# Performance work log

Measured on AMD Instinct MI355X. Metric: run time of the kernel, lower is better.

Reference implementation:

```python
import jax, jax.numpy as jnp
import numpy as np

KEY_DIM = 32
D = 128  # attn_ratio * key_dim
H = 8
DIM = 512
N = 1024
B = 16
EPS = 1e-5


def setup_inputs() -> dict:
    key = jax.random.key(0)
    ks = jax.random.split(key, 5)
    x = jax.random.normal(ks[0], (B, DIM, N), dtype=jnp.float32)
    # grouped Conv1d(dim -> H*(2*key_dim+d), k=1, groups=H): per-group weight [H, 192, 64]
    qkv_w = jax.random.normal(ks[1], (H, 2 * KEY_DIM + D, DIM // H), dtype=jnp.float32) * 0.05
    qkv_b = jax.random.normal(ks[2], (H, 2 * KEY_DIM + D), dtype=jnp.float32) * 0.02
    # proj Conv1d(d*H -> dim, k=1)
    proj_w = jax.random.normal(ks[3], (DIM, D * H), dtype=jnp.float32) * 0.03
    proj_b = jax.random.normal(ks[4], (DIM,), dtype=jnp.float32) * 0.02
    bn_gamma = jnp.ones((DIM,), dtype=jnp.float32)
    bn_beta = jnp.zeros((DIM,), dtype=jnp.float32)
    bn_mean = jnp.zeros((DIM,), dtype=jnp.float32)
    bn_var = jnp.ones((DIM,), dtype=jnp.float32)
    return {"x": x, "qkv_w": qkv_w, "qkv_b": qkv_b, "proj_w": proj_w,
            "proj_b": proj_b, "bn_gamma": bn_gamma, "bn_beta": bn_beta,
            "bn_mean": bn_mean, "bn_var": bn_var}


def reference(x, qkv_w, qkv_b, proj_w, proj_b, bn_gamma, bn_beta, bn_mean, bn_var):
    Bx, C, Nx = x.shape
    scale = KEY_DIM ** (-0.5)
    # grouped 1x1 conv: split channels into H groups of C//H
    xh = x.reshape(Bx, H, C // H, Nx)                      # [B,H,Cg,N]
    qkv = jnp.einsum('bhcn,hoc->bhon', xh, qkv_w) + qkv_b[None, :, :, None]
    q, k, v = jnp.split(qkv, [KEY_DIM, 2 * KEY_DIM], axis=2)  # [B,H,kd,N],[B,H,kd,N],[B,H,d,N]
    # attn[m,n] = sum_c q[c,m]*k[c,n]
    attn = jnp.einsum('bhcm,bhcn->bhmn', q, k) * scale      # [B,H,N,N]
    attn = jax.nn.softmax(attn, axis=-1)
    # out[d,m] = sum_n v[d,n]*attn[m,n]  (v @ attn^T)
    o = jnp.einsum('bhdn,bhmn->bhdm', v, attn)              # [B,H,d,N]
    o = o.reshape(Bx, H * D, Nx)
    # proj: ReLU -> 1x1 conv -> BatchNorm1d (inference mode)
    o = jax.nn.relu(o)
    o = jnp.einsum('bcn,oc->bon', o, proj_w) + proj_b[None, :, None]
    inv = bn_gamma / jnp.sqrt(bn_var + EPS)
    o = o * inv[None, :, None] + (bn_beta - bn_mean * inv)[None, :, None]
    return o
```

## Files before the change

### kernel.cpp

```cpp
#include <hip/hip_runtime.h>
#include <math.h>

typedef unsigned short u16;
typedef unsigned int u32;

#define Bb   16
#define Hh   8
#define KD   32
#define DV   128
#define DIM  512
#define Nn   1024
#define OQKV 192
#define SCALE2 0.25503490221320355f

typedef short bf16x8 __attribute__((ext_vector_type(8)));
typedef float f32x16 __attribute__((ext_vector_type(16)));

#define MFMA32(a, b, c) __builtin_amdgcn_mfma_f32_32x32x16_bf16(a, b, c, 0, 0, 0)

__device__ __forceinline__ float fexp2(float x) {
#if __has_builtin(__builtin_amdgcn_exp2f)
  return __builtin_amdgcn_exp2f(x);
#else
  return exp2f(x);
#endif
}

__device__ __forceinline__ u16 f2bf_rn(float f) {
  return (u16)((__float_as_uint(f) + 0x8000u) >> 16);
}

#if __has_builtin(__builtin_amdgcn_cvt_pk_bf16_f32)
__device__ __forceinline__ u32 pk2(float lo, float hi) {
  auto r = __builtin_amdgcn_cvt_pk_bf16_f32(lo, hi);
  return __builtin_bit_cast(u32, r);
}
#else
__device__ __forceinline__ u32 pk2(float lo, float hi) {
  u32 a = __float_as_uint(lo) + 0x8000u;
  u32 b = __float_as_uint(hi) + 0x8000u;
  return __builtin_amdgcn_perm(b, a, 0x07060302);
}
#endif

#if __has_builtin(__builtin_amdgcn_permlane32_swap)
__device__ __forceinline__ void pswap(u32& a, u32& b) {
  auto r = __builtin_amdgcn_permlane32_swap(a, b, false, false);
  a = r[0]; b = r[1];
}
#else
__device__ __forceinline__ void pswap(u32& a, u32& b) {
  asm("v_permlane32_swap_b32 %0, %1" : "+v"(a), "+v"(b));
}
#endif

__global__ __launch_bounds__(256) void prep_kernel(
    const float* __restrict__ pw, const float* __restrict__ qw,
    const float* __restrict__ pb, const float* __restrict__ g,
    const float* __restrict__ bt, const float* __restrict__ mn,
    const float* __restrict__ vr, u16* __restrict__ Wb,
    u16* __restrict__ Wq, float* __restrict__ invA, float* __restrict__ addB) {
  const int tid = blockIdx.x * 256 + threadIdx.x;
  {
    float4 v = *(const float4*)&pw[(size_t)tid * 4];
    uint2 pk; pk.x = pk2(v.x, v.y); pk.y = pk2(v.z, v.w);
    *(uint2*)&Wb[(size_t)tid * 4] = pk;
  }
  if (tid < 24576) {
    float4 v = *(const float4*)&qw[(size_t)tid * 4];
    uint2 pk; pk.x = pk2(v.x, v.y); pk.y = pk2(v.z, v.w);
    *(uint2*)&Wq[(size_t)tid * 4] = pk;
  }
  if (tid < DIM) {
    float inv = g[tid] * rsqrtf(vr[tid] + 1e-5f);
    invA[tid] = inv;
    addB[tid] = pb[tid] * inv + bt[tid] - mn[tid] * inv;
  }
}

__global__ __launch_bounds__(256) void qkv_kernel(
    const float* __restrict__ x, const u16* __restrict__ Wq,
    const float* __restrict__ bias, u16* __restrict__ Qb,
    u16* __restrict__ Kb, u16* __restrict__ Vb) {
  const int nt = blockIdx.x, bh = blockIdx.y;
  const int b = bh >> 3, h = bh & 7;
  const int tid = threadIdx.x;
  const int wid = tid >> 6, lane = tid & 63;
  const int r32 = lane & 31, hh = lane >> 5;
  const int n0 = nt * 128;

  __shared__ __align__(16) u16 Ws[192 * 72];
  __shared__ __align__(16) u16 Xs[128 * 72];

  const u16* wqp = Wq + (size_t)h * OQKV * 64;
  #pragma unroll
  for (int i = 0; i < 6; ++i) {
    int idx = i * 256 + tid;
    int o = idx >> 3, c8 = (idx & 7) * 8;
    *(uint4*)&Ws[o * 72 + c8] = *(const uint4*)&wqp[o * 64 + c8];
  }
  const float* xp = x + ((size_t)b * DIM + h * 64) * Nn + n0;
  #pragma unroll
  for (int i = 0; i < 4; ++i) {
    int idx = i * 256 + tid;
    int cp = idx >> 5, n4 = (idx & 31) * 4;
    const int c = 2 * cp;
    float4 a = *(const float4*)&xp[(size_t)c * Nn + n4];
    float4 d = *(const float4*)&xp[(size_t)(c + 1) * Nn + n4];
    *(u32*)&Xs[(n4 + 0) * 72 + c] = pk2(a.x, d.x);
    *(u32*)&Xs[(n4 + 1) * 72 + c] = pk2(a.y, d.y);
    *(u32*)&Xs[(n4 + 2) * 72 + c] = pk2(a.z, d.z);
    *(u32*)&Xs[(n4 + 3) * 72 + c] = pk2(a.w, d.w);
  }
  __syncthreads();

  f32x16 acc[6];
  #pragma unroll
  for (int t = 0; t < 6; ++t)
    #pragma unroll
    for (int r = 0; r < 16; ++r) acc[t][r] = 0.0f;

  const int nw = wid * 32;
  #pragma unroll
  for (int k = 0; k < 4; ++k) {
    const int ko = k * 16 + hh * 8;
    bf16x8 xb = *(const bf16x8*)&Xs[(nw + r32) * 72 + ko];
    #pragma unroll
    for (int t = 0; t < 6; ++t) {
      bf16x8 wa = *(const bf16x8*)&Ws[(t * 32 + r32) * 72 + ko];
      acc[t] = MFMA32(wa, xb, acc[t]);
    }
  }

  const int n = n0 + nw + r32;
  const float* bp = bias + h * OQKV;
  #pragma unroll
  for (int t = 0; t < 6; ++t) {
    #pragma unroll
    for (int g = 0; g < 4; ++g) {
      const int ob = t * 32 + 8 * g + 4 * hh;
      float4 bv = *(const float4*)&bp[ob];
      float v0 = acc[t][4 * g + 0] + bv.x;
      float v1 = acc[t][4 * g + 1] + bv.y;
      float v2 = acc[t][4 * g + 2] + bv.z;
      float v3 = acc[t][4 * g + 3] + bv.w;
      if (t == 0) {
        uint2 pk;
        pk.x = pk2(v0 * SCALE2, v1 * SCALE2);
        pk.y = pk2(v2 * SCALE2, v3 * SCALE2);
        *(uint2*)&Qb[((size_t)bh * Nn + n) * 32 + ob] = pk;
      } else if (t == 1) {
        uint2 pk; pk.x = pk2(v0, v1); pk.y = pk2(v2, v3);
        *(uint2*)&Kb[((size_t)bh * Nn + n) * 32 + ob - 32] = pk;
      } else {
        const int d = ob - 64;
        Vb[((size_t)bh * DV + d + 0) * Nn + n] = f2bf_rn(v0);
        Vb[((size_t)bh * DV + d + 1) * Nn + n] = f2bf_rn(v1);
        Vb[((size_t)bh * DV + d + 2) * Nn + n] = f2bf_rn(v2);
        Vb[((size_t)bh * DV + d + 3) * Nn + n] = f2bf_rn(v3);
      }
    }
  }
}

__global__ __launch_bounds__(256) void attn_kernel(
    const u16* __restrict__ Qb, const u16* __restrict__ Kb,
    const u16* __restrict__ Vb, u16* __restrict__ Ot) {
  const int blk = blockIdx.x;
  const int xcd = blk & 7, j = blk >> 3;
  const int bh = (xcd << 4) | (j >> 3);
  const int mt = j & 7;
  const int tid = threadIdx.x;
  const int wid = tid >> 6, lane = tid & 63;
  const int r32 = lane & 31, hh = lane >> 5;
  const int mw = mt * 128 + wid * 32;

  __shared__ __align__(16) u16 Vs[2][128 * 72];

  const u16* qp = Qb + ((size_t)bh * Nn + mw + r32) * 32;
  const bf16x8 qb0 = *(const bf16x8*)&qp[hh * 8];
  const bf16x8 qb1 = *(const bf16x8*)&qp[16 + hh * 8];

  const u16* kbase = Kb + (size_t)bh * Nn * 32;
  const u16* vbase = Vb + (size_t)bh * DV * Nn;

  int sd[4], sn[4];
  #pragma unroll
  for (int i = 0; i < 4; ++i) {
    int idx = i * 256 + tid;
    sd[i] = idx >> 3; sn[i] = (idx & 7) * 8;
  }

  uint4 vreg[4];
  #pragma unroll
  for (int i = 0; i < 4; ++i)
    vreg[i] = *(const uint4*)&vbase[(size_t)sd[i] * Nn + sn[i]];
  #pragma unroll
  for (int i = 0; i < 4; ++i)
    *(uint4*)&Vs[0][sd[i] * 72 + sn[i]] = vreg[i];

  bf16x8 ka[4];
  {
    const u16* kp0 = kbase + (size_t)r32 * 32;
    const u16* kp1 = kbase + (size_t)(32 + r32) * 32;
    ka[0] = *(const bf16x8*)&kp0[hh * 8];
    ka[1] = *(const bf16x8*)&kp0[16 + hh * 8];
    ka[2] = *(const bf16x8*)&kp1[hh * 8];
    ka[3] = *(const bf16x8*)&kp1[16 + hh * 8];
  }

  f32x16 o[4];
  #pragma unroll
  for (int t = 0; t < 4; ++t)
    #pragma unroll
    for (int r = 0; r < 16; ++r) o[t][r] = 0.0f;
  float lsum = 0.0f;

  for (int ch = 0; ch < 16; ++ch) {
    const int n0 = ch * 64;
    const int p = ch & 1;
    __syncthreads();

    if (ch < 15) {
      #pragma unroll
      for (int i = 0; i < 4; ++i)
        vreg[i] = *(const uint4*)&vbase[(size_t)sd[i] * Nn + n0 + 64 + sn[i]];
    }

    f32x16 c0, c1;
    #pragma unroll
    for (int r = 0; r < 16; ++r) { c0[r] = 0.0f; c1[r] = 0.0f; }
    __builtin_amdgcn_s_setprio(1);
    c0 = MFMA32(ka[0], qb0, c0);
    c0 = MFMA32(ka[1], qb1, c0);
    c1 = MFMA32(ka[2], qb0, c1);
    c1 = MFMA32(ka[3], qb1, c1);
    __builtin_amdgcn_s_setprio(0);

    bf16x8 kn[4];
    if (ch < 15) {
      const u16* kp0 = kbase + (size_t)(n0 + 64 + r32) * 32;
      const u16* kp1 = kbase + (size_t)(n0 + 96 + r32) * 32;
      kn[0] = *(const bf16x8*)&kp0[hh * 8];
      kn[1] = *(const bf16x8*)&kp0[16 + hh * 8];
      kn[2] = *(const bf16x8*)&kp1[hh * 8];
      kn[3] = *(const bf16x8*)&kp1[16 + hh * 8];
    }

    float csum = 0.0f;
    #pragma unroll
    for (int r = 0; r < 16; ++r) { c0[r] = fexp2(c0[r]); csum += c0[r]; }
    #pragma unroll
    for (int r = 0; r < 16; ++r) { c1[r] = fexp2(c1[r]); csum += c1[r]; }
    lsum += csum;

    u32 Pk[16];
    #pragma unroll
    for (int g = 0; g < 4; ++g) {
      Pk[2 * g]     = pk2(c0[4 * g + 0], c0[4 * g + 1]);
      Pk[2 * g + 1] = pk2(c0[4 * g + 2], c0[4 * g + 3]);
      Pk[8 + 2 * g]     = pk2(c1[4 * g + 0], c1[4 * g + 1]);
      Pk[8 + 2 * g + 1] = pk2(c1[4 * g + 2], c1[4 * g + 3]);
    }
    pswap(Pk[0], Pk[2]);   pswap(Pk[1], Pk[3]);
    pswap(Pk[4], Pk[6]);   pswap(Pk[5], Pk[7]);
    pswap(Pk[8], Pk[10]);  pswap(Pk[9], Pk[11]);
    pswap(Pk[12], Pk[14]); pswap(Pk[13], Pk[15]);

    union { u32 d[4]; bf16x8 v; } pb[4];
    #pragma unroll
    for (int i = 0; i < 4; ++i) {
      pb[i].d[0] = Pk[4 * i + 0];
      pb[i].d[1] = Pk[4 * i + 1];
      pb[i].d[2] = Pk[4 * i + 2];
      pb[i].d[3] = Pk[4 * i + 3];
    }

    __builtin_amdgcn_s_setprio(1);
    #pragma unroll
    for (int t = 0; t < 4; ++t) {
      const u16* vrow = &Vs[p][(t * 32 + r32) * 72];
      #pragma unroll
      for (int s = 0; s < 4; ++s) {
        bf16x8 va = *(const bf16x8*)&vrow[s * 16 + hh * 8];
        o[t] = MFMA32(va, pb[s].v, o[t]);
      }
    }
    __builtin_amdgcn_s_setprio(0);

    if (ch < 15) {
      #pragma unroll
      for (int i = 0; i < 4; ++i)
        *(uint4*)&Vs[1 - p][sd[i] * 72 + sn[i]] = vreg[i];
      #pragma unroll
      for (int i = 0; i < 4; ++i) ka[i] = kn[i];
    }
  }

  lsum += __shfl_xor(lsum, 32, 64);
  const float inv = 1.0f / lsum;
  const int m = mw + r32;
  const int b = bh >> 3, h = bh & 7;
  u16* obase = Ot + ((size_t)b * Nn + m) * 1024 + h * DV + 4 * hh;
  #pragma unroll
  for (int t = 0; t < 4; ++t) {
    #pragma unroll
    for (int g = 0; g < 4; ++g) {
      float v0 = fmaxf(o[t][4 * g + 0] * inv, 0.0f);
      float v1 = fmaxf(o[t][4 * g + 1] * inv, 0.0f);
      float v2 = fmaxf(o[t][4 * g + 2] * inv, 0.0f);
      float v3 = fmaxf(o[t][4 * g + 3] * inv, 0.0f);
      uint2 pk; pk.x = pk2(v0, v1); pk.y = pk2(v2, v3);
      *(uint2*)&obase[t * 32 + 8 * g] = pk;
    }
  }
}

__global__ __launch_bounds__(256) void proj_kernel(
    const u16* __restrict__ Ot, const u16* __restrict__ Wb,
    const float* __restrict__ invA, const float* __restrict__ addB,
    float* __restrict__ out) {
  const int blk = blockIdx.x;
  const int xcd = blk & 7, rr = blk >> 3;
  const int pairl = rr >> 2, oct = rr & 3;
  const int pair = xcd * 16 + pairl;
  const int b = pair >> 3, nt = pair & 7;
  const int n0 = nt * 128, oc0 = oct * 128;
  const int tid = threadIdx.x;
  const int wid = tid >> 6, lane = tid & 63;
  const int r32 = lane & 31, hh = lane >> 5;
  const int ocw = (wid >> 1) * 64, nw = (wid & 1) * 64;

  __shared__ __align__(16) u16 Ws[128 * 72];
  __shared__ __align__(16) u16 Os[128 * 72];

  f32x16 o[2][2];
  #pragma unroll
  for (int t = 0; t < 2; ++t)
    #pragma unroll
    for (int u = 0; u < 2; ++u)
      #pragma unroll
      for (int r = 0; r < 16; ++r) o[t][u][r] = 0.0f;

  for (int ic0 = 0; ic0 < 1024; ic0 += 64) {
    __syncthreads();
    #pragma unroll
    for (int i = 0; i < 4; ++i) {
      int idx = i * 256 + tid;
      int row = idx >> 3, c8 = (idx & 7) * 8;
      *(uint4*)&Ws[row * 72 + c8] =
          *(const uint4*)&Wb[(size_t)(oc0 + row) * 1024 + ic0 + c8];
    }
    #pragma unroll
    for (int i = 0; i < 4; ++i) {
      int idx = i * 256 + tid;
      int row = idx >> 3, c8 = (idx & 7) * 8;
      *(uint4*)&Os[row * 72 + c8] =
          *(const uint4*)&Ot[((size_t)b * Nn + n0 + row) * 1024 + ic0 + c8];
    }
    __syncthreads();

    #pragma unroll
    for (int s = 0; s < 4; ++s) {
      const int ko = s * 16 + hh * 8;
      bf16x8 a0 = *(const bf16x8*)&Ws[(ocw + r32) * 72 + ko];
      bf16x8 a1 = *(const bf16x8*)&Ws[(ocw + 32 + r32) * 72 + ko];
      bf16x8 b0 = *(const bf16x8*)&Os[(nw + r32) * 72 + ko];
      bf16x8 b1 = *(const bf16x8*)&Os[(nw + 32 + r32) * 72 + ko];
      o[0][0] = MFMA32(a0, b0, o[0][0]);
      o[0][1] = MFMA32(a0, b1, o[0][1]);
      o[1][0] = MFMA32(a1, b0, o[1][0]);
      o[1][1] = MFMA32(a1, b1, o[1][1]);
    }
  }

  #pragma unroll
  for (int t = 0; t < 2; ++t) {
    const int obase = oc0 + ocw + t * 32 + 4 * hh;
    #pragma unroll
    for (int g = 0; g < 4; ++g) {
      const int oc = obase + 8 * g;
      float4 iv = *(const float4*)&invA[oc];
      float4 av = *(const float4*)&addB[oc];
      #pragma unroll
      for (int u = 0; u < 2; ++u) {
        const int n = n0 + nw + u * 32 + r32;
        out[((size_t)b * DIM + oc + 0) * Nn + n] = o[t][u][4 * g + 0] * iv.x + av.x;
        out[((size_t)b * DIM + oc + 1) * Nn + n] = o[t][u][4 * g + 1] * iv.y + av.y;
        out[((size_t)b * DIM + oc + 2) * Nn + n] = o[t][u][4 * g + 2] * iv.z + av.z;
        out[((size_t)b * DIM + oc + 3) * Nn + n] = o[t][u][4 * g + 3] * iv.w + av.w;
      }
    }
  }
}

extern "C" void kernel_launch(void* const* d_in, const int* in_sizes, int n_in,
                              void* d_out, int out_size, void* d_ws,
                              size_t ws_size, hipStream_t stream) {
  const float* x      = (const float*)d_in[0];
  const float* qkv_w  = (const float*)d_in[1];
  const float* qkv_b  = (const float*)d_in[2];
  const float* proj_w = (const float*)d_in[3];
  const float* proj_b = (const float*)d_in[4];
  const float* bn_g   = (const float*)d_in[5];
  const float* bn_b   = (const float*)d_in[6];
  const float* bn_m   = (const float*)d_in[7];
  const float* bn_v   = (const float*)d_in[8];
  float* out = (float*)d_out;

  char* ws = (char*)d_ws;
  u16* Qb   = (u16*)(ws);
  u16* Kb   = (u16*)(ws + 8388608);
  u16* Vb   = (u16*)(ws + 16777216);
  u16* Ot   = (u16*)(ws + 50331648);
  u16* Wb   = (u16*)(ws + 83886080);
  u16* Wq   = (u16*)(ws + 84934656);
  float* invA = (float*)(ws + 85131264);
  float* addB = (float*)(ws + 85133312);

  prep_kernel<<<dim3(512), 256, 0, stream>>>(
      proj_w, qkv_w, proj_b, bn_g, bn_b, bn_m, bn_v, Wb, Wq, invA, addB);
  qkv_kernel<<<dim3(8, Bb * Hh), 256, 0, stream>>>(x, Wq, qkv_b, Qb, Kb, Vb);
  attn_kernel<<<dim3(1024), 256, 0, stream>>>(Qb, Kb, Vb, Ot);
  proj_kernel<<<dim3(512), 256, 0, stream>>>(Ot, Wb, invA, addB, out);
}
```

Baseline: 190.8 us.

## Software-pipeline QK^T and exp of next chunk against PV MFMAs

Restructures the attention loop so the QK^T MFMAs and exp/pack of chunk ch+1 are issued alongside the PV MFMAs of chunk ch. The first S tile is computed in a prologue and the last PV pass runs in an epilogue. The aim is to hide the softmax VALU work and the dependent MFMA latency behind matrix work. The cost is more live registers (the packed P tile stays resident). The last iteration also prefetches K rows past N, which are never used but may read out of bounds for the final head.

Measured after the change: 188.3 us. Within noise of the previous version (-1.3%).

```diff
diff --git a/kernel.cpp b/kernel.cpp
--- a/kernel.cpp
+++ b/kernel.cpp
@@ -208,6 +208,22 @@
     ka[2] = *(const bf16x8*)&kp1[hh * 8];
     ka[3] = *(const bf16x8*)&kp1[16 + hh * 8];
   }
+  f32x16 c0, c1;
+  #pragma unroll
+  for (int r = 0; r < 16; ++r) { c0[r] = 0.0f; c1[r] = 0.0f; }
+  c0 = MFMA32(ka[0], qb0, c0);
+  c0 = MFMA32(ka[1], qb1, c0);
+  c1 = MFMA32(ka[2], qb0, c1);
+  c1 = MFMA32(ka[3], qb1, c1);
+
+  {
+    const u16* kp0 = kbase + (size_t)(64 + r32) * 32;
+    const u16* kp1 = kbase + (size_t)(96 + r32) * 32;
+    ka[0] = *(const bf16x8*)&kp0[hh * 8];
+    ka[1] = *(const bf16x8*)&kp0[16 + hh * 8];
+    ka[2] = *(const bf16x8*)&kp1[hh * 8];
+    ka[3] = *(const bf16x8*)&kp1[16 + hh * 8];
+  }
 
   f32x16 o[4];
   #pragma unroll
@@ -215,46 +231,16 @@
     #pragma unroll
     for (int r = 0; r < 16; ++r) o[t][r] = 0.0f;
   float lsum = 0.0f;
-
-  for (int ch = 0; ch < 16; ++ch) {
-    const int n0 = ch * 64;
-    const int p = ch & 1;
-    __syncthreads();
-
-    if (ch < 15) {
-      #pragma unroll
-      for (int i = 0; i < 4; ++i)
-        vreg[i] = *(const uint4*)&vbase[(size_t)sd[i] * Nn + n0 + 64 + sn[i]];
-    }
-
-    f32x16 c0, c1;
-    #pragma unroll
-    for (int r = 0; r < 16; ++r) { c0[r] = 0.0f; c1[r] = 0.0f; }
-    __builtin_amdgcn_s_setprio(1);
-    c0 = MFMA32(ka[0], qb0, c0);
-    c0 = MFMA32(ka[1], qb1, c0);
-    c1 = MFMA32(ka[2], qb0, c1);
-    c1 = MFMA32(ka[3], qb1, c1);
-    __builtin_amdgcn_s_setprio(0);
-
-    bf16x8 kn[4];
-    if (ch < 15) {
-      const u16* kp0 = kbase + (size_t)(n0 + 64 + r32) * 32;
-      const u16* kp1 = kbase + (size_t)(n0 + 96 + r32) * 32;
-      kn[0] = *(const bf16x8*)&kp0[hh * 8];
-      kn[1] = *(const bf16x8*)&kp0[16 + hh * 8];
-      kn[2] = *(const bf16x8*)&kp1[hh * 8];
-      kn[3] = *(const bf16x8*)&kp1[16 + hh * 8];
-    }
-
+  u32 Pk[16];
+  union { u32 d[4]; bf16x8 v; } pbf[4];
+
+  auto finishS = [&]() {
     float csum = 0.0f;
     #pragma unroll
     for (int r = 0; r < 16; ++r) { c0[r] = fexp2(c0[r]); csum += c0[r]; }
     #pragma unroll
     for (int r = 0; r < 16; ++r) { c1[r] = fexp2(c1[r]); csum += c1[r]; }
     lsum += csum;
-
-    u32 Pk[16];
     #pragma unroll
     for (int g = 0; g < 4; ++g) {
       Pk[2 * g]     = pk2(c0[4 * g + 0], c0[4 * g + 1]);
@@ -266,36 +252,76 @@
     pswap(Pk[4], Pk[6]);   pswap(Pk[5], Pk[7]);
     pswap(Pk[8], Pk[10]);  pswap(Pk[9], Pk[11]);
     pswap(Pk[12], Pk[14]); pswap(Pk[13], Pk[15]);
-
-    union { u32 d[4]; bf16x8 v; } pb[4];
     #pragma unroll
     for (int i = 0; i < 4; ++i) {
-      pb[i].d[0] = Pk[4 * i + 0];
-      pb[i].d[1] = Pk[4 * i + 1];
-      pb[i].d[2] = Pk[4 * i + 2];
-      pb[i].d[3] = Pk[4 * i + 3];
-    }
+      pbf[i].d[0] = Pk[4 * i + 0];
+      pbf[i].d[1] = Pk[4 * i + 1];
+      pbf[i].d[2] = Pk[4 * i + 2];
+      pbf[i].d[3] = Pk[4 * i + 3];
+    }
+  };
+
+  finishS();
+
+  for (int ch = 0; ch < 15; ++ch) {
+    const int p = ch & 1;
+    __syncthreads();
+
+    #pragma unroll
+    for (int i = 0; i < 4; ++i)
+      vreg[i] = *(const uint4*)&vbase[(size_t)sd[i] * Nn + (ch + 1) * 64 + sn[i]];
 
     __builtin_amdgcn_s_setprio(1);
+    #pragma unroll
+    for (int r = 0; r < 16; ++r) { c0[r] = 0.0f; c1[r] = 0.0f; }
+    c0 = MFMA32(ka[0], qb0, c0);
+    c0 = MFMA32(ka[1], qb1, c0);
+    c1 = MFMA32(ka[2], qb0, c1);
+    c1 = MFMA32(ka[3], qb1, c1);
+
+    bf16x8 kn[4];
+    {
+      const u16* kp0 = kbase + (size_t)((ch + 2) * 64 + r32) * 32;
+      const u16* kp1 = kbase + (size_t)((ch + 2) * 64 + 32 + r32) * 32;
+      kn[0] = *(const bf16x8*)&kp0[hh * 8];
+      kn[1] = *(const bf16x8*)&kp0[16 + hh * 8];
+      kn[2] = *(const bf16x8*)&kp1[hh * 8];
+      kn[3] = *(const bf16x8*)&kp1[16 + hh * 8];
+    }
+
     #pragma unroll
     for (int t = 0; t < 4; ++t) {
       const u16* vrow = &Vs[p][(t * 32 + r32) * 72];
       #pragma unroll
       for (int s = 0; s < 4; ++s) {
         bf16x8 va = *(const bf16x8*)&vrow[s * 16 + hh * 8];
-        o[t] = MFMA32(va, pb[s].v, o[t]);
+        o[t] = MFMA32(va, pbf[s].v, o[t]);
       }
     }
     __builtin_amdgcn_s_setprio(0);
 
-    if (ch < 15) {
-      #pragma unroll
-      for (int i = 0; i < 4; ++i)
-        *(uint4*)&Vs[1 - p][sd[i] * 72 + sn[i]] = vreg[i];
-      #pragma unroll
-      for (int i = 0; i < 4; ++i) ka[i] = kn[i];
-    }
-  }
+    #pragma unroll
+    for (int i = 0; i < 4; ++i)
+      *(uint4*)&Vs[1 - p][sd[i] * 72 + sn[i]] = vreg[i];
+
+    finishS();
+
+    #pragma unroll
+    for (int i = 0; i < 4; ++i) ka[i] = kn[i];
+  }
+
+  __syncthreads();
+  __builtin_amdgcn_s_setprio(1);
+  #pragma unroll
+  for (int t = 0; t < 4; ++t) {
+    const u16* vrow = &Vs[1][(t * 32 + r32) * 72];
+    #pragma unroll
+    for (int s = 0; s < 4; ++s) {
+      bf16x8 va = *(const bf16x8*)&vrow[s * 16 + hh * 8];
+      o[t] = MFMA32(va, pbf[s].v, o[t]);
+    }
+  }
+  __builtin_amdgcn_s_setprio(0);
 
   lsum += __shfl_xor(lsum, 32, 64);
   const float inv = 1.0f / lsum;
```
